# Kernel optimization log

Measured on AMD Instinct MI355X. Metric: run time of the kernel, lower is better.

Reference implementation:

```python
import jax, jax.numpy as jnp
import numpy as np

B, C_IN, C_OUT, E, H, W = 64, 384, 384, 8, 28, 28


def setup_inputs() -> dict:
    key = jax.random.key(0)
    k1, k2, k3 = jax.random.split(key, 3)
    x = jax.random.normal(k1, (B, C_IN, H, W), dtype=jnp.float32)
    routing_weights = jax.random.uniform(k2, (B, E), dtype=jnp.float32)
    # kaiming_normal_(mode='fan_out') per expert: std = sqrt(2 / fan_out), fan_out = out_channels * 1 * 1
    std = float(np.sqrt(2.0 / C_OUT))
    weight = jax.random.normal(k3, (E, C_OUT, C_IN), dtype=jnp.float32) * std
    return {"x": x, "routing_weights": routing_weights, "weight": weight}


def reference(x, routing_weights, weight):
    # Per-sample aggregated 1x1 conv weights: [b, c_out, c_in]
    agg = jnp.einsum('be,eoi->boi', routing_weights, weight)
    # Per-sample channel mixing (1x1 conv with groups=b == batched GEMM)
    out = jnp.einsum('boi,bihw->bohw', agg, x)
    return out
```

## Files before the change

### kernel.cpp

```cpp
#include <hip/hip_runtime.h>
#include <cstdint>

#define B_   64
#define CI_  384
#define CO_  384
#define HW_  784
#define E_   8
#define G_   (CI_ / 8)

typedef unsigned short ushort_t;
typedef unsigned int   uint_t;

typedef __attribute__((ext_vector_type(8))) short bf16x8;
typedef __attribute__((ext_vector_type(4))) float f32x4;

__device__ __forceinline__ ushort_t f2bf_rne(float f) {
  uint_t u = __builtin_bit_cast(uint_t, f);
  u += 0x7fffu + ((u >> 16) & 1u);
  return (ushort_t)(u >> 16);
}

__device__ __forceinline__ uint_t pack_bf16_trunc(float f0, float f1) {
  return __builtin_amdgcn_perm(__builtin_bit_cast(uint_t, f1),
                               __builtin_bit_cast(uint_t, f0),
                               0x07060302u);
}

#define AGG_BLOCKS 288
#define XQ_BLOCKS  (G_ * B_)

__global__ __launch_bounds__(256) void prep(const float* __restrict__ rw,
                                            const float* __restrict__ w,
                                            const float* __restrict__ x,
                                            ushort_t* __restrict__ agg,
                                            ushort_t* __restrict__ xq) {
  __shared__ float r[B_ * E_];
  const int blk = blockIdx.x;
  const int tid = threadIdx.x;

  if (blk < AGG_BLOCKS) {
    r[tid]       = rw[tid];
    r[tid + 256] = rw[tid + 256];
    const int base = blk * 512 + tid * 2;
    float2 wv[E_];
#pragma unroll
    for (int e = 0; e < E_; ++e)
      wv[e] = *(const float2*)&w[e * (CO_ * CI_) + base];
    __syncthreads();
#pragma unroll 8
    for (int b = 0; b < B_; ++b) {
      float ax = 0.f, ay = 0.f;
#pragma unroll
      for (int e = 0; e < E_; ++e) {
        const float rv = r[b * E_ + e];
        ax += rv * wv[e].x;
        ay += rv * wv[e].y;
      }
      const uint_t v = (uint_t)f2bf_rne(ax) | ((uint_t)f2bf_rne(ay) << 16);
      *(uint_t*)&agg[(size_t)b * (CO_ * CI_) + base] = v;
    }
  } else {
    const int idx = blk - AGG_BLOCKS;
    const int g = idx % G_;
    const int b = idx / G_;
    const float* xp = x + ((size_t)b * CI_ + g * 8) * HW_;
    ushort_t* op = xq + (((size_t)b * G_ + g) * HW_) * 8;
#pragma unroll
    for (int c = 0; c < 4; ++c) {
      const int hw = c * 256 + tid;
      if (hw < HW_) {
        float v[8];
#pragma unroll
        for (int j = 0; j < 8; ++j) v[j] = xp[(size_t)j * HW_ + hw];
        uint4 u;
        u.x = pack_bf16_trunc(v[0], v[1]);
        u.y = pack_bf16_trunc(v[2], v[3]);
        u.z = pack_bf16_trunc(v[4], v[5]);
        u.w = pack_bf16_trunc(v[6], v[7]);
        *(uint4*)&op[hw * 8] = u;
      }
    }
  }
}

#define TM 48
#define TN 112
#define KIT 12

__global__ __launch_bounds__(64, 2) void moe_gemm2(const ushort_t* __restrict__ Agg,
                                                   const ushort_t* __restrict__ Xq,
                                                   float* __restrict__ Out) {
  const int lane = threadIdx.x;
  const int l15 = lane & 15;
  const int lq  = lane >> 4;

  const int bx = blockIdx.x;
  const int by = blockIdx.y;
  const int bg  = by / 56;
  const int rem = by - bg * 56;
  const int mt  = rem / 7;
  const int nt  = rem - mt * 7;
  const int b   = bg * 8 + bx;

  const ushort_t* Abase = Agg + (size_t)b * CO_ * CI_ + (size_t)(mt * TM + l15) * CI_ + lq * 8;
  const ushort_t* Bbase = Xq + (((size_t)b * G_ + lq) * HW_ + (nt * TN + l15)) * 8;

  f32x4 acc[3][7];
#pragma unroll
  for (int i = 0; i < 3; ++i)
#pragma unroll
    for (int j = 0; j < 7; ++j)
      acc[i][j] = (f32x4)0.f;

  bf16x8 A0[3], A1[3], A2[3], B0[7], B1[7], B2[7];

#define LA(dst, KK)                                                            \
  {                                                                            \
    _Pragma("unroll") for (int mf_ = 0; mf_ < 3; ++mf_)                        \
        dst[mf_] = *(const bf16x8*)(Abase + (KK) * 32 + mf_ * (16 * CI_));     \
  }
#define LB(dst, KK)                                                            \
  {                                                                            \
    _Pragma("unroll") for (int nf_ = 0; nf_ < 7; ++nf_)                        \
        dst[nf_] = *(const bf16x8*)(Bbase + (KK) * (4 * HW_ * 8) + nf_ * 128); \
  }
#define MM(A_, B_)                                                             \
  {                                                                            \
    _Pragma("unroll") for (int mf_ = 0; mf_ < 3; ++mf_)                        \
        _Pragma("unroll") for (int nf_ = 0; nf_ < 7; ++nf_)                    \
            acc[mf_][nf_] = __builtin_amdgcn_mfma_f32_16x16x32_bf16(           \
                A_[mf_], B_[nf_], acc[mf_][nf_], 0, 0, 0);                     \
  }

  LA(A0, 0); LB(B0, 0);
  LA(A1, 1); LB(B1, 1);
  LA(A2, 2); LB(B2, 2);

#pragma unroll 1
  for (int t = 0; t < 9; t += 3) {
    MM(A0, B0); LA(A0, t + 3); LB(B0, t + 3);
    MM(A1, B1); LA(A1, t + 4); LB(B1, t + 4);
    MM(A2, B2); LA(A2, t + 5); LB(B2, t + 5);
  }
  MM(A0, B0);
  MM(A1, B1);
  MM(A2, B2);

  float* Ob = Out + (size_t)b * CO_ * HW_;
#pragma unroll
  for (int mf = 0; mf < 3; ++mf) {
#pragma unroll
    for (int nf = 0; nf < 7; ++nf) {
      const int n = nt * TN + nf * 16 + l15;
      const int mbase = mt * TM + mf * 16 + lq * 4;
#pragma unroll
      for (int r = 0; r < 4; ++r)
        Ob[(size_t)(mbase + r) * HW_ + n] = acc[mf][nf][r];
    }
  }
}

extern "C" void kernel_launch(void* const* d_in, const int* in_sizes, int n_in,
                              void* d_out, int out_size, void* d_ws, size_t ws_size,
                              hipStream_t stream) {
  const float* x  = (const float*)d_in[0];
  const float* rw = (const float*)d_in[1];
  const float* w  = (const float*)d_in[2];
  float* out = (float*)d_out;

  ushort_t* agg = (ushort_t*)d_ws;
  ushort_t* xq  = agg + (size_t)B_ * CO_ * CI_;

  prep<<<AGG_BLOCKS + XQ_BLOCKS, 256, 0, stream>>>(rw, w, x, agg, xq);
  moe_gemm2<<<dim3(8, 448), 64, 0, stream>>>(agg, xq, out);
}
```

Before: 176.2 us.

## Replace register-only GEMM with LDS-staged 128x128 tiles using global_load_lds double buffering

Switches the batched GEMM from single-wave 48x112 tiles loaded straight from global memory into registers to 256-thread blocks computing 128x128 tiles. Operands are staged into double-buffered LDS with an XOR swizzle via direct global-to-LDS loads. The aim is more reuse of A and B fragments across four waves and less redundant global traffic. In exchange it pads the HW dimension (784 is not a multiple of 128), which wastes about 12% of compute, and adds a barrier on every K step.

```diff
diff --git a/kernel.cpp b/kernel.cpp
--- a/kernel.cpp
+++ b/kernel.cpp
@@ -83,79 +83,113 @@
   }
 }
 
-#define TM 48
-#define TN 112
-#define KIT 12
-
-__global__ __launch_bounds__(64, 2) void moe_gemm2(const ushort_t* __restrict__ Agg,
-                                                   const ushort_t* __restrict__ Xq,
-                                                   float* __restrict__ Out) {
-  const int lane = threadIdx.x;
-  const int l15 = lane & 15;
-  const int lq  = lane >> 4;
+#define BM 128
+#define BN 128
+#define BK 32
+#define KIT (CI_ / BK)
+
+__global__ __launch_bounds__(256, 4) void moe_gemm3(const ushort_t* __restrict__ Agg,
+                                                    const ushort_t* __restrict__ Xq,
+                                                    float* __restrict__ Out) {
+  __shared__ __align__(16) ushort_t As[2][BM * BK];
+  __shared__ __align__(16) ushort_t Bs[2][BN * BK];
+
+  const int tid  = threadIdx.x;
+  const int lane = tid & 63;
+  const int wave = tid >> 6;
+  const int wm = wave & 1, wn = wave >> 1;
 
   const int bx = blockIdx.x;
   const int by = blockIdx.y;
-  const int bg  = by / 56;
-  const int rem = by - bg * 56;
+  const int bg  = by / 21;
+  const int rem = by - bg * 21;
   const int mt  = rem / 7;
   const int nt  = rem - mt * 7;
   const int b   = bg * 8 + bx;
 
-  const ushort_t* Abase = Agg + (size_t)b * CO_ * CI_ + (size_t)(mt * TM + l15) * CI_ + lq * 8;
-  const ushort_t* Bbase = Xq + (((size_t)b * G_ + lq) * HW_ + (nt * TN + l15)) * 8;
-
-  f32x4 acc[3][7];
-#pragma unroll
-  for (int i = 0; i < 3; ++i)
-#pragma unroll
-    for (int j = 0; j < 7; ++j)
+  const int sr0 = tid >> 2,          sq0 = (tid & 3) ^ ((tid >> 3) & 3);
+  const int sr1 = (tid + 256) >> 2,  sq1 = (tid & 3) ^ (((tid + 256) >> 3) & 3);
+
+  const ushort_t* Ab = Agg + (size_t)b * CO_ * CI_ + (size_t)(mt * BM) * CI_;
+  const ushort_t* Asrc0 = Ab + sr0 * CI_ + sq0 * 8;
+  const ushort_t* Asrc1 = Ab + sr1 * CI_ + sq1 * 8;
+
+  int hw0 = nt * BN + sr0; hw0 = hw0 < HW_ ? hw0 : HW_ - 1;
+  int hw1 = nt * BN + sr1; hw1 = hw1 < HW_ ? hw1 : HW_ - 1;
+  const ushort_t* Xb = Xq + (size_t)b * G_ * HW_ * 8;
+  const ushort_t* Bsrc0 = Xb + ((size_t)sq0 * HW_ + hw0) * 8;
+  const ushort_t* Bsrc1 = Xb + ((size_t)sq1 * HW_ + hw1) * 8;
+
+  const int l15 = lane & 15;
+  const int lq  = lane >> 4;
+  const int xqA = lq ^ ((l15 >> 1) & 3);
+
+  f32x4 acc[4][4];
+#pragma unroll
+  for (int i = 0; i < 4; ++i)
+#pragma unroll
+    for (int j = 0; j < 4; ++j)
       acc[i][j] = (f32x4)0.f;
 
-  bf16x8 A0[3], A1[3], A2[3], B0[7], B1[7], B2[7];
-
-#define LA(dst, KK)                                                            \
+#define STAGE(PB, KK)                                                          \
   {                                                                            \
-    _Pragma("unroll") for (int mf_ = 0; mf_ < 3; ++mf_)                        \
-        dst[mf_] = *(const bf16x8*)(Abase + (KK) * 32 + mf_ * (16 * CI_));     \
-  }
-#define LB(dst, KK)                                                            \
-  {                                                                            \
-    _Pragma("unroll") for (int nf_ = 0; nf_ < 7; ++nf_)                        \
-        dst[nf_] = *(const bf16x8*)(Bbase + (KK) * (4 * HW_ * 8) + nf_ * 128); \
-  }
-#define MM(A_, B_)                                                             \
-  {                                                                            \
-    _Pragma("unroll") for (int mf_ = 0; mf_ < 3; ++mf_)                        \
-        _Pragma("unroll") for (int nf_ = 0; nf_ < 7; ++nf_)                    \
-            acc[mf_][nf_] = __builtin_amdgcn_mfma_f32_16x16x32_bf16(           \
-                A_[mf_], B_[nf_], acc[mf_][nf_], 0, 0, 0);                     \
-  }
-
-  LA(A0, 0); LB(B0, 0);
-  LA(A1, 1); LB(B1, 1);
-  LA(A2, 2); LB(B2, 2);
+    __builtin_amdgcn_global_load_lds(                                          \
+        (const __attribute__((address_space(1))) uint_t*)(Asrc0 + (KK) * BK),  \
+        (__attribute__((address_space(3))) uint_t*)&As[PB][tid * 8], 16, 0, 0);\
+    __builtin_amdgcn_global_load_lds(                                          \
+        (const __attribute__((address_space(1))) uint_t*)(Asrc1 + (KK) * BK),  \
+        (__attribute__((address_space(3))) uint_t*)&As[PB][(tid + 256) * 8],   \
+        16, 0, 0);                                                             \
+    const size_t bo_ = (size_t)(KK) * (4 * HW_ * 8);                           \
+    __builtin_amdgcn_global_load_lds(                                          \
+        (const __attribute__((address_space(1))) uint_t*)(Bsrc0 + bo_),        \
+        (__attribute__((address_space(3))) uint_t*)&Bs[PB][tid * 8], 16, 0, 0);\
+    __builtin_amdgcn_global_load_lds(                                          \
+        (const __attribute__((address_space(1))) uint_t*)(Bsrc1 + bo_),        \
+        (__attribute__((address_space(3))) uint_t*)&Bs[PB][(tid + 256) * 8],   \
+        16, 0, 0);                                                             \
+  }
+
+  STAGE(0, 0);
+  __syncthreads();
 
 #pragma unroll 1
-  for (int t = 0; t < 9; t += 3) {
-    MM(A0, B0); LA(A0, t + 3); LB(B0, t + 3);
-    MM(A1, B1); LA(A1, t + 4); LB(B1, t + 4);
-    MM(A2, B2); LA(A2, t + 5); LB(B2, t + 5);
-  }
-  MM(A0, B0);
-  MM(A1, B1);
-  MM(A2, B2);
+  for (int kk = 0; kk < KIT; ++kk) {
+    const int buf = kk & 1;
+    if (kk + 1 < KIT) STAGE(1 - buf, kk + 1);
+
+    bf16x8 a[4], bb[4];
+#pragma unroll
+    for (int mf = 0; mf < 4; ++mf) {
+      const int row = wm * 64 + mf * 16 + l15;
+      a[mf] = *(const bf16x8*)&As[buf][(row * 4 + xqA) * 8];
+    }
+#pragma unroll
+    for (int nf = 0; nf < 4; ++nf) {
+      const int col = wn * 64 + nf * 16 + l15;
+      bb[nf] = *(const bf16x8*)&Bs[buf][(col * 4 + xqA) * 8];
+    }
+#pragma unroll
+    for (int mf = 0; mf < 4; ++mf)
+#pragma unroll
+      for (int nf = 0; nf < 4; ++nf)
+        acc[mf][nf] = __builtin_amdgcn_mfma_f32_16x16x32_bf16(a[mf], bb[nf],
+                                                              acc[mf][nf], 0, 0, 0);
+    __syncthreads();
+  }
 
   float* Ob = Out + (size_t)b * CO_ * HW_;
 #pragma unroll
-  for (int mf = 0; mf < 3; ++mf) {
-#pragma unroll
-    for (int nf = 0; nf < 7; ++nf) {
-      const int n = nt * TN + nf * 16 + l15;
-      const int mbase = mt * TM + mf * 16 + lq * 4;
-#pragma unroll
-      for (int r = 0; r < 4; ++r)
-        Ob[(size_t)(mbase + r) * HW_ + n] = acc[mf][nf][r];
+  for (int mf = 0; mf < 4; ++mf) {
+#pragma unroll
+    for (int nf = 0; nf < 4; ++nf) {
+      const int n = nt * BN + wn * 64 + nf * 16 + l15;
+      if (n < HW_) {
+        const int mbase = mt * BM + wm * 64 + mf * 16 + lq * 4;
+#pragma unroll
+        for (int r = 0; r < 4; ++r)
+          Ob[(size_t)(mbase + r) * HW_ + n] = acc[mf][nf][r];
+      }
     }
   }
 }
@@ -172,5 +206,5 @@
   ushort_t* xq  = agg + (size_t)B_ * CO_ * CI_;
 
   prep<<<AGG_BLOCKS + XQ_BLOCKS, 256, 0, stream>>>(rw, w, x, agg, xq);
-  moe_gemm2<<<dim3(8, 448), 64, 0, stream>>>(agg, xq, out);
-}
+  moe_gemm3<<<dim3(8, 21 * (B_ / 8)), 256, 0, stream>>>(agg, xq, out);
+}
```

After: 173.6 us. No clear change (-1.5%).

## Restructure batched GEMM into 12-wave blocks with LDS staging via global_load_lds

Applied to the files above, without the earlier changes.

Replaces the single-wave register-direct GEMM with 768-thread blocks that each compute the full 384 output channels for a 112-column tile. A and B tiles are loaded straight into LDS with global_load_lds, in a swizzled layout, with double and triple buffering and explicit vmcnt waits plus barriers. Each x tile is now loaded once per block instead of once per 48-row M-tile, which cuts redundant global traffic. The cost is barrier synchronisation, LDS pressure and reliance on precise waitcnt handling.

```diff
diff --git a/kernel.cpp b/kernel.cpp
--- a/kernel.cpp
+++ b/kernel.cpp
@@ -13,6 +13,9 @@
 
 typedef __attribute__((ext_vector_type(8))) short bf16x8;
 typedef __attribute__((ext_vector_type(4))) float f32x4;
+
+#define AS1 __attribute__((address_space(1)))
+#define AS3 __attribute__((address_space(3)))
 
 __device__ __forceinline__ ushort_t f2bf_rne(float f) {
   uint_t u = __builtin_bit_cast(uint_t, f);
@@ -83,79 +86,120 @@
   }
 }
 
-#define TM 48
 #define TN 112
-#define KIT 12
-
-__global__ __launch_bounds__(64, 2) void moe_gemm2(const ushort_t* __restrict__ Agg,
-                                                   const ushort_t* __restrict__ Xq,
-                                                   float* __restrict__ Out) {
-  const int lane = threadIdx.x;
-  const int l15 = lane & 15;
-  const int lq  = lane >> 4;
+#define BK 32
+#define KIT (CI_ / BK)
+
+__global__ __launch_bounds__(768, 4) void moe_gemm6(const ushort_t* __restrict__ Xq,
+                                                    const ushort_t* __restrict__ Agg,
+                                                    float* __restrict__ Out) {
+  __shared__ __align__(16) ushort_t As[2][CO_ * BK];
+  __shared__ __align__(16) ushort_t Bs[3][TN * BK];
+
+  const int tid  = threadIdx.x;
+  const int lane = tid & 63;
+  const int w    = tid >> 6;
+  const int l15  = lane & 15;
+  const int lq   = lane >> 4;
+  const int xqA  = lq ^ ((l15 >> 1) & 3);
 
   const int bx = blockIdx.x;
   const int by = blockIdx.y;
-  const int bg  = by / 56;
-  const int rem = by - bg * 56;
-  const int mt  = rem / 7;
-  const int nt  = rem - mt * 7;
-  const int b   = bg * 8 + bx;
-
-  const ushort_t* Abase = Agg + (size_t)b * CO_ * CI_ + (size_t)(mt * TM + l15) * CI_ + lq * 8;
-  const ushort_t* Bbase = Xq + (((size_t)b * G_ + lq) * HW_ + (nt * TN + l15)) * 8;
-
-  f32x4 acc[3][7];
-#pragma unroll
-  for (int i = 0; i < 3; ++i)
+  const int bg = by / 7;
+  const int nt = by - bg * 7;
+  const int b  = bg * 8 + bx;
+
+  const int sq0 = (tid & 3) ^ ((tid >> 3) & 3);
+  const int sr0 = tid >> 2;
+  const ushort_t* Ab = Agg + (size_t)b * CO_ * CI_;
+  const ushort_t* Asrc0 = Ab + sr0 * CI_ + sq0 * 8;
+  const ushort_t* Asrc1 = Ab + (sr0 + 192) * CI_ + sq0 * 8;
+
+  const int bcol = tid >> 2;
+  const int bq   = (tid & 3) ^ ((tid >> 3) & 3);
+  const ushort_t* Xb = Xq + (size_t)b * G_ * HW_ * 8;
+  const ushort_t* Bsrc = Xb + ((size_t)bq * HW_ + nt * TN + bcol) * 8;
+
+  f32x4 acc[2][7];
+#pragma unroll
+  for (int i = 0; i < 2; ++i)
 #pragma unroll
     for (int j = 0; j < 7; ++j)
       acc[i][j] = (f32x4)0.f;
 
-  bf16x8 A0[3], A1[3], A2[3], B0[7], B1[7], B2[7];
-
-#define LA(dst, KK)                                                            \
-  {                                                                            \
-    _Pragma("unroll") for (int mf_ = 0; mf_ < 3; ++mf_)                        \
-        dst[mf_] = *(const bf16x8*)(Abase + (KK) * 32 + mf_ * (16 * CI_));     \
-  }
-#define LB(dst, KK)                                                            \
-  {                                                                            \
-    _Pragma("unroll") for (int nf_ = 0; nf_ < 7; ++nf_)                        \
-        dst[nf_] = *(const bf16x8*)(Bbase + (KK) * (4 * HW_ * 8) + nf_ * 128); \
-  }
-#define MM(A_, B_)                                                             \
-  {                                                                            \
-    _Pragma("unroll") for (int mf_ = 0; mf_ < 3; ++mf_)                        \
-        _Pragma("unroll") for (int nf_ = 0; nf_ < 7; ++nf_)                    \
-            acc[mf_][nf_] = __builtin_amdgcn_mfma_f32_16x16x32_bf16(           \
-                A_[mf_], B_[nf_], acc[mf_][nf_], 0, 0, 0);                     \
-  }
-
-  LA(A0, 0); LB(B0, 0);
-  LA(A1, 1); LB(B1, 1);
-  LA(A2, 2); LB(B2, 2);
-
-#pragma unroll 1
-  for (int t = 0; t < 9; t += 3) {
-    MM(A0, B0); LA(A0, t + 3); LB(B0, t + 3);
-    MM(A1, B1); LA(A1, t + 4); LB(B1, t + 4);
-    MM(A2, B2); LA(A2, t + 5); LB(B2, t + 5);
-  }
-  MM(A0, B0);
-  MM(A1, B1);
-  MM(A2, B2);
-
-  float* Ob = Out + (size_t)b * CO_ * HW_;
-#pragma unroll
-  for (int mf = 0; mf < 3; ++mf) {
+#define STAGE_A(PB, KK)                                                        \
+  {                                                                            \
+    __builtin_amdgcn_global_load_lds(                                          \
+        (const AS1 uint_t*)(Asrc0 + (KK) * BK),                                \
+        (AS3 uint_t*)&As[PB][tid * 8], 16, 0, 0);                              \
+    __builtin_amdgcn_global_load_lds(                                          \
+        (const AS1 uint_t*)(Asrc1 + (KK) * BK),                                \
+        (AS3 uint_t*)&As[PB][(tid + 768) * 8], 16, 0, 0);                      \
+  }
+
+#define STAGE_B(PB, KK)                                                        \
+  {                                                                            \
+    if (tid < 448)                                                             \
+      __builtin_amdgcn_global_load_lds(                                        \
+          (const AS1 uint_t*)(Bsrc + (size_t)(KK) * (4 * HW_ * 8)),            \
+          (AS3 uint_t*)&Bs[PB][tid * 8], 16, 0, 0);                            \
+  }
+
+#define COMPUTE(AB, BB)                                                        \
+  {                                                                            \
+    bf16x8 a[2], bb[7];                                                        \
+    _Pragma("unroll") for (int mf = 0; mf < 2; ++mf) {                         \
+      const int row = w * 32 + mf * 16 + l15;                                  \
+      a[mf] = *(const bf16x8*)&As[AB][(row * 4 + xqA) * 8];                    \
+    }                                                                          \
+    _Pragma("unroll") for (int nf = 0; nf < 7; ++nf) {                         \
+      const int col = nf * 16 + l15;                                           \
+      bb[nf] = *(const bf16x8*)&Bs[BB][(col * 4 + xqA) * 8];                   \
+    }                                                                          \
+    __builtin_amdgcn_s_setprio(1);                                             \
+    _Pragma("unroll") for (int mf = 0; mf < 2; ++mf)                           \
+      _Pragma("unroll") for (int nf = 0; nf < 7; ++nf)                         \
+        acc[mf][nf] = __builtin_amdgcn_mfma_f32_16x16x32_bf16(a[mf], bb[nf],   \
+                                                              acc[mf][nf],     \
+                                                              0, 0, 0);        \
+    __builtin_amdgcn_s_setprio(0);                                             \
+  }
+
+#define WAITV(N7)                                                              \
+  {                                                                            \
+    if (w < 7) { asm volatile("s_waitcnt vmcnt(" N7 ")" ::: "memory"); }       \
+    else       { asm volatile("s_waitcnt vmcnt(0)" ::: "memory"); }            \
+  }
+
+#define BODY(T, N7)                                                            \
+  {                                                                            \
+    WAITV(N7);                                                                 \
+    __builtin_amdgcn_s_barrier();                                              \
+    __builtin_amdgcn_sched_barrier(0);                                         \
+    if ((T) + 1 < KIT) STAGE_A(((T) + 1) & 1, (T) + 1);                        \
+    if ((T) + 2 < KIT) STAGE_B(((T) + 2) % 3, (T) + 2);                        \
+    COMPUTE((T) & 1, (T) % 3);                                                 \
+    __builtin_amdgcn_sched_barrier(0);                                         \
+  }
+
+  STAGE_B(0, 0);
+  STAGE_A(0, 0);
+  STAGE_B(1, 1);
+
+  BODY(0,  "1") BODY(1,  "1") BODY(2,  "1") BODY(3,  "1")
+  BODY(4,  "1") BODY(5,  "1") BODY(6,  "1") BODY(7,  "1")
+  BODY(8,  "1") BODY(9,  "1") BODY(10, "1") BODY(11, "0")
+
+  float* Ob = Out + (size_t)b * CO_ * HW_ + nt * TN;
+#pragma unroll
+  for (int mf = 0; mf < 2; ++mf) {
 #pragma unroll
     for (int nf = 0; nf < 7; ++nf) {
-      const int n = nt * TN + nf * 16 + l15;
-      const int mbase = mt * TM + mf * 16 + lq * 4;
+      const int n  = nf * 16 + l15;
+      const int mb = w * 32 + mf * 16 + lq * 4;
 #pragma unroll
       for (int r = 0; r < 4; ++r)
-        Ob[(size_t)(mbase + r) * HW_ + n] = acc[mf][nf][r];
+        Ob[(size_t)(mb + r) * HW_ + n] = acc[mf][nf][r];
     }
   }
 }
@@ -172,5 +216,5 @@
   ushort_t* xq  = agg + (size_t)B_ * CO_ * CI_;
 
   prep<<<AGG_BLOCKS + XQ_BLOCKS, 256, 0, stream>>>(rw, w, x, agg, xq);
-  moe_gemm2<<<dim3(8, 448), 64, 0, stream>>>(agg, xq, out);
-}
+  moe_gemm6<<<dim3(8, 7 * (B_ / 8)), 768, 0, stream>>>(xq, agg, out);
+}
```

After: 174.2 us. About the same (-1.2%).
